# Performance work log

Measured on AMD Instinct MI355X. Metric: run time of the kernel, lower is better.

## Reference

```python
import jax, jax.numpy as jnp
import numpy as np

B, IN_CH, OUT_CH, T, N_STATE, FACTOR = 8, 128, 128, 16384, 256, 2
DT = 1.0
LN_EPS = 1e-5


def setup_inputs() -> dict:
    key = jax.random.key(0)
    k = jax.random.split(key, 5)
    x = jax.random.normal(k[0], (B, IN_CH, T), jnp.float32)
    raw_lambda = jnp.zeros((N_STATE,), jnp.float32)
    B_c = jax.random.normal(k[1], (IN_CH, N_STATE), jnp.float32) * (1.0 / np.sqrt(IN_CH))
    C_mat = jax.random.normal(k[2], (N_STATE, OUT_CH), jnp.float32) * (1.0 / np.sqrt(N_STATE))
    ln_gamma = jnp.ones((OUT_CH,), jnp.float32)
    ln_beta = jnp.zeros((OUT_CH,), jnp.float32)
    # Conv1d(out_ch*factor, out_ch, kernel_size=1): weight (out, in), bias (out,)
    W = jax.random.normal(k[3], (OUT_CH, OUT_CH * FACTOR), jnp.float32) * (1.0 / np.sqrt(OUT_CH * FACTOR))
    b = jax.random.normal(k[4], (OUT_CH,), jnp.float32) * 0.01
    return {"x": x, "raw_lambda": raw_lambda, "B_c": B_c, "C_mat": C_mat,
            "ln_gamma": ln_gamma, "ln_beta": ln_beta, "W": W, "b": b}


def reference(x, raw_lambda, B_c, C_mat, ln_gamma, ln_beta, W, b):
    # --- SSMLayerZOH ---
    lam = -jax.nn.softplus(raw_lambda)              # (N,) continuous diag, < 0
    A_d = jnp.exp(lam * DT)                         # ZOH discretized diag
    B_d = B_c * ((A_d - 1.0) / lam)[None, :]        # (IN, N)
    v = jnp.einsum('bct,cn->tbn', x, B_d)           # per-step input injection

    def step(s, vt):
        s = s * A_d + vt
        return s, s

    s0 = jnp.zeros((x.shape[0], lam.shape[0]), x.dtype)
    _, ss = jax.lax.scan(step, s0, v)               # (T, B, N)
    y = jnp.einsum('tbn,no->bto', ss, C_mat)        # (B, T, OUT)

    # --- LayerNorm(out_ch) + SiLU ---
    mu = jnp.mean(y, axis=-1, keepdims=True)
    var = jnp.mean((y - mu) ** 2, axis=-1, keepdims=True)
    h = (y - mu) / jnp.sqrt(var + LN_EPS) * ln_gamma + ln_beta
    h = h * jax.nn.sigmoid(h)                       # SiLU

    # --- Resample (factor > 1 branch): downsample T, stack factor into channels ---
    h = jnp.transpose(h, (0, 2, 1))                 # (B, OUT, T)
    Bn, C, Tt = h.shape
    hr = h.reshape(Bn, C, Tt // FACTOR, FACTOR)
    hr = jnp.transpose(hr, (0, 1, 3, 2)).reshape(Bn, C * FACTOR, Tt // FACTOR)
    out = jnp.einsum('bct,oc->bot', hr, W) + b[None, :, None]  # conv1x1
    return out
```

## Files before the change

kernel.cpp:

```cpp
#include <hip/hip_runtime.h>

#define BATCH 8
#define CIN 128
#define OCH 128
#define T_LEN 16384
#define NS 256
#define CHUNK 64
#define NCHUNK (T_LEN / CHUNK)
#define THALF (T_LEN / 2)
#define SCHUNK 8192
#define HROW 132
#define NCHK 4

typedef __attribute__((ext_vector_type(8))) short bf16x8;
typedef __attribute__((ext_vector_type(4))) float f32x4;
typedef __attribute__((ext_vector_type(4))) unsigned int u32x4;

__device__ __forceinline__ unsigned int pk2(float lo, float hi) {
  unsigned int d;
  asm("v_cvt_pk_bf16_f32 %0, %1, %2" : "=v"(d) : "v"(lo), "v"(hi));
  return d;
}
__device__ __forceinline__ unsigned short f2bf(float f) {
  unsigned int u = __float_as_uint(f);
  u += 0x7fffu + ((u >> 16) & 1u);
  return (unsigned short)(u >> 16);
}
__device__ __forceinline__ float softplusf_(float v) {
  return (v > 20.0f) ? v : log1pf(expf(v));
}
__device__ __forceinline__ void rawbar() {
  __builtin_amdgcn_sched_barrier(0);
  asm volatile("s_waitcnt lgkmcnt(0)" ::: "memory");
  __builtin_amdgcn_sched_barrier(0);
  __builtin_amdgcn_s_barrier();
  __builtin_amdgcn_sched_barrier(0);
}

__global__ __launch_bounds__(256) void k_prep(
    const float* __restrict__ rl, const float* __restrict__ Bc,
    const float* __restrict__ Cm, const float* __restrict__ W,
    unsigned short* __restrict__ BdT, unsigned short* __restrict__ CT,
    unsigned short* __restrict__ Wb, float* __restrict__ Ad, float* __restrict__ rL,
    float* __restrict__ PWf)
{
  const int tid = blockIdx.x * 256 + threadIdx.x;
  if (tid < NS * CIN) {
    const int n = tid >> 7, c = tid & 127;
    float lam = -softplusf_(rl[n]);
    float ad = expf(lam);
    float sc = (ad - 1.0f) / lam;
    BdT[tid] = f2bf(Bc[c * NS + n] * sc);
  } else if (tid < 2 * NS * CIN) {
    const int i = tid - NS * CIN;
    const int o = i >> 8, n = i & 255;
    CT[i] = f2bf(Cm[n * OCH + o]);
  } else if (tid < 3 * NS * CIN) {
    const int i = tid - 2 * NS * CIN;
    Wb[i] = f2bf(W[i]);
  } else if (tid < 3 * NS * CIN + NS) {
    const int n = tid - 3 * NS * CIN;
    float lam = -softplusf_(rl[n]);
    Ad[n] = expf(lam);
    rL[n] = expf(lam * (float)CHUNK);
  } else if (tid < 3 * NS * CIN + NS + 32 * NS) {
    const int i = tid - (3 * NS * CIN + NS);
    const int tp = i >> 8, n = i & 255;
    float lam = -softplusf_(rl[n]);
    PWf[i] = expf(lam * (float)(2 * tp + 1));
  }
}

__global__ __launch_bounds__(256) void k_combine(float* __restrict__ carry,
                                                 const float* __restrict__ rL)
{
  const int b = blockIdx.x >> 3;
  const int ng = blockIdx.x & 7;
  const int t = threadIdx.x;
  __shared__ float Y[32][NCHUNK];
  float* base = carry + ((size_t)b * NCHUNK + t) * NS + ng * 32;
  #pragma unroll
  for (int i4 = 0; i4 < 8; ++i4) {
    float4 q = *(const float4*)(base + i4 * 4);
    Y[i4 * 4 + 0][t] = q.x; Y[i4 * 4 + 1][t] = q.y;
    Y[i4 * 4 + 2][t] = q.z; Y[i4 * 4 + 3][t] = q.w;
  }
  float rp[32];
  #pragma unroll
  for (int i = 0; i < 32; ++i) rp[i] = rL[ng * 32 + i];
  __syncthreads();
  for (int d = 1; d < NCHUNK; d <<= 1) {
    float tmp[32];
    #pragma unroll
    for (int i = 0; i < 32; ++i) tmp[i] = (t >= d) ? Y[i][t - d] : 0.0f;
    __syncthreads();
    #pragma unroll
    for (int i = 0; i < 32; ++i) { Y[i][t] += rp[i] * tmp[i]; rp[i] *= rp[i]; }
    __syncthreads();
  }
  const int tm = (t == 0) ? 0 : (t - 1);
  #pragma unroll
  for (int i4 = 0; i4 < 8; ++i4) {
    float a = Y[i4 * 4 + 0][tm], bb = Y[i4 * 4 + 1][tm];
    float c = Y[i4 * 4 + 2][tm], dd = Y[i4 * 4 + 3][tm];
    float4 q;
    q.x = (t == 0) ? 0.0f : a;  q.y = (t == 0) ? 0.0f : bb;
    q.z = (t == 0) ? 0.0f : c;  q.w = (t == 0) ? 0.0f : dd;
    *(float4*)(base + i4 * 4) = q;
  }
}

__global__ __launch_bounds__(512, 4) void k_scan(
    const float* __restrict__ x,
    const unsigned short* __restrict__ BdT,
    const float* __restrict__ Ad,
    unsigned int* __restrict__ s0,
    float* __restrict__ carry)
{
  const int bid = blockIdx.x;
  const int b = bid >> 8;
  const int kc = bid & 255;
  const int tid = threadIdx.x;
  const int w = tid >> 6, l = tid & 63, l15 = l & 15, g = l >> 4;

  __shared__ __align__(16) unsigned int Xt[64 * 64];

  {
    const int c2 = w * 8 + (l & 7);
    const int t0b = (l >> 3) * 8;
    const float* r0 = x + ((size_t)(b * CIN + 2 * c2)) * T_LEN + kc * CHUNK + t0b;
    const f32x4 xa0 = *(const f32x4*)r0;
    const f32x4 xa1 = *(const f32x4*)(r0 + 4);
    const f32x4 xb0 = *(const f32x4*)(r0 + T_LEN);
    const f32x4 xb1 = *(const f32x4*)(r0 + T_LEN + 4);
    #pragma unroll
    for (int k = 0; k < 8; ++k) {
      const int t = t0b + k;
      const float va = (k < 4) ? xa0[k & 3] : xa1[k & 3];
      const float vb = (k < 4) ? xb0[k & 3] : xb1[k & 3];
      Xt[t * 64 + (c2 ^ ((t & 7) << 2))] = pk2(va, vb);
    }
  }

  bf16x8 Bf[2][4];
  #pragma unroll
  for (int nt = 0; nt < 2; ++nt)
    #pragma unroll
    for (int kt = 0; kt < 4; ++kt)
      Bf[nt][kt] = *(const bf16x8*)&BdT[(w * 32 + nt * 16 + l15) * CIN + kt * 32 + g * 8];

  float A1[2], A2[2], A3[2], A4[2], A8[2], A16[2], A4G[2], M1[2], M2[2];
  #pragma unroll
  for (int nt = 0; nt < 2; ++nt) {
    const float a1 = Ad[w * 32 + nt * 16 + l15];
    A1[nt] = a1; A2[nt] = a1 * a1; A3[nt] = A2[nt] * a1; A4[nt] = A2[nt] * A2[nt];
    A8[nt] = A4[nt] * A4[nt]; A16[nt] = A8[nt] * A8[nt];
    float a4g = 1.0f;
    if (g & 1) a4g *= A4[nt];
    if (g & 2) a4g *= A8[nt];
    A4G[nt] = a4g;
    M1[nt] = (g >= 1) ? A4[nt] : 0.0f;
    M2[nt] = (g >= 2) ? A8[nt] : 0.0f;
  }
  __syncthreads();

  f32x4 vac[4][2] = {};
  #pragma unroll
  for (int kt = 0; kt < 4; ++kt) {
    bf16x8 afr[4];
    #pragma unroll
    for (int mt = 0; mt < 4; ++mt)
      afr[mt] = *(const bf16x8*)&Xt[(mt * 16 + l15) * 64 + ((kt * 16 + g * 4) ^ ((l15 & 7) << 2))];
    #pragma unroll
    for (int nt = 0; nt < 2; ++nt)
      #pragma unroll
      for (int mt = 0; mt < 4; ++mt)
        vac[mt][nt] = __builtin_amdgcn_mfma_f32_16x16x32_bf16(afr[mt], Bf[nt][kt], vac[mt][nt], 0, 0, 0);
  }

  float crv[2];
  #pragma unroll
  for (int nt = 0; nt < 2; ++nt) {
    float cr = 0.0f;
    #pragma unroll
    for (int mt = 0; mt < 4; ++mt) {
      const float p0 = vac[mt][nt][0];
      const float p1 = fmaf(A1[nt], p0, vac[mt][nt][1]);
      const float p2 = fmaf(A1[nt], p1, vac[mt][nt][2]);
      const float p3 = fmaf(A1[nt], p2, vac[mt][nt][3]);
      float c0 = p3;
      float u = __shfl_up(c0, 16);
      c0 = fmaf(M1[nt], u, c0);
      u = __shfl_up(c0, 32);
      c0 = fmaf(M2[nt], u, c0);
      float e = __shfl_up(c0, 16);
      e = (g == 0) ? 0.0f : e;
      const float seed = fmaf(A4G[nt], cr, e);
      vac[mt][nt][0] = fmaf(A1[nt], seed, p0);
      vac[mt][nt][1] = fmaf(A2[nt], seed, p1);
      vac[mt][nt][2] = fmaf(A3[nt], seed, p2);
      vac[mt][nt][3] = fmaf(A4[nt], seed, p3);
      const float ctop = __shfl(c0, 48 + l15);
      cr = fmaf(A16[nt], cr, ctop);
    }
    crv[nt] = cr;
  }

  unsigned int* sc = s0 + (size_t)(b * NCHUNK + kc) * SCHUNK;
  #pragma unroll
  for (int mt = 0; mt < 4; ++mt)
    #pragma unroll
    for (int nt = 0; nt < 2; ++nt) {
      const int n = w * 32 + nt * 16 + l15;
      #pragma unroll
      for (int rp = 0; rp < 2; ++rp) {
        const int tp = mt * 8 + g * 2 + rp;
        sc[tp * 256 + n] = pk2(vac[mt][nt][rp * 2], vac[mt][nt][rp * 2 + 1]);
      }
    }
  if (g == 0) {
    #pragma unroll
    for (int nt = 0; nt < 2; ++nt)
      carry[((size_t)b * NCHUNK + kc) * NS + (w * 32 + nt * 16 + l15)] = crv[nt];
  }
}

__global__ __launch_bounds__(512, 2) void k_apply(
    const unsigned int* __restrict__ S,
    const unsigned short* __restrict__ CT,
    const unsigned short* __restrict__ Wb,
    const float* __restrict__ PWf,
    const float* __restrict__ Ad,
    const float* __restrict__ carry,
    const float* __restrict__ lng, const float* __restrict__ lnb,
    const float* __restrict__ bias,
    float* __restrict__ out)
{
  const int bid = blockIdx.x;
  const int b = bid / (NCHUNK / NCHK);
  const int kc0 = (bid % (NCHUNK / NCHK)) * NCHK;
  const int tid = threadIdx.x;
  const int w = tid >> 6, l = tid & 63, l15 = l & 15, g = l >> 4;
  const int tt = w >> 2, oq = w & 3;

  __shared__ __align__(16) unsigned short V2[64 * 256];
  __shared__ __align__(16) unsigned int Hr[32 * HROW];
  __shared__ __align__(16) float Lexf[64 * 8];

  const f32x4 adv = *(const f32x4*)&Ad[4 * l];

  bf16x8 ctf[8][2];
  #pragma unroll
  for (int kt = 0; kt < 8; ++kt)
    #pragma unroll
    for (int ot = 0; ot < 2; ++ot)
      ctf[kt][ot] = *(const bf16x8*)&CT[(oq * 32 + ot * 16 + l15) * NS + kt * 32 + g * 8];
  bf16x8 wf[8];
  #pragma unroll
  for (int kt = 0; kt < 8; ++kt)
    wf[kt] = *(const bf16x8*)&Wb[(w * 16 + l15) * NS + kt * 32 + g * 8];
  f32x4 pwv[4];
  #pragma unroll
  for (int r = 0; r < 4; ++r)
    pwv[r] = *(const f32x4*)&PWf[(r * 8 + w) * 256 + 4 * l];
  const float ga0 = lng[oq * 32 + l15],      be0 = lnb[oq * 32 + l15];
  const float ga1 = lng[oq * 32 + 16 + l15], be1 = lnb[oq * 32 + 16 + l15];
  const float bia = bias[w * 16 + l15];

  u32x4 st0, st1, st2, st3;
  f32x4 sd;

#define LOAD_ST(KC) do {                                                    \
    const unsigned int* scb_ = S + (size_t)(b * NCHUNK + (KC)) * SCHUNK;    \
    st0 = *(const u32x4*)&scb_[0 * 2048 + tid * 4];                         \
    st1 = *(const u32x4*)&scb_[1 * 2048 + tid * 4];                         \
    st2 = *(const u32x4*)&scb_[2 * 2048 + tid * 4];                         \
    st3 = *(const u32x4*)&scb_[3 * 2048 + tid * 4];                         \
    sd  = *(const f32x4*)&carry[((size_t)b * NCHUNK + (KC)) * NS + 4 * l];  \
  } while (0)

#define CORRECT_ROW(QV, RR) do {                                            \
    const float e00 = sd[0] * pwv[RR][0];                                   \
    const float e01 = sd[1] * pwv[RR][1];                                   \
    const float e02 = sd[2] * pwv[RR][2];                                   \
    const float e03 = sd[3] * pwv[RR][3];                                   \
    const float lo0 = __uint_as_float(QV[0] << 16) + e00;                   \
    const float hi0 = __uint_as_float(QV[0] & 0xffff0000u) + e00 * adv[0];  \
    const float lo1 = __uint_as_float(QV[1] << 16) + e01;                   \
    const float hi1 = __uint_as_float(QV[1] & 0xffff0000u) + e01 * adv[1];  \
    const float lo2 = __uint_as_float(QV[2] << 16) + e02;                   \
    const float hi2 = __uint_as_float(QV[2] & 0xffff0000u) + e02 * adv[2];  \
    const float lo3 = __uint_as_float(QV[3] << 16) + e03;                   \
    const float hi3 = __uint_as_float(QV[3] & 0xffff0000u) + e03 * adv[3];  \
    const int t0_ = ((RR) * 8 + w) * 2;                                     \
    const int t1_ = t0_ + 1;                                                \
    uint2 wlo; wlo.x = pk2(lo0, lo1); wlo.y = pk2(lo2, lo3);                \
    uint2 whi; whi.x = pk2(hi0, hi1); whi.y = pk2(hi2, hi3);                \
    *(uint2*)&V2[t0_ * 256 + ((((l >> 1) ^ ((t0_ & 7) << 2)) << 3) | ((l & 1) << 2))] = wlo; \
    *(uint2*)&V2[t1_ * 256 + ((((l >> 1) ^ ((t1_ & 7) << 2)) << 3) | ((l & 1) << 2))] = whi; \
  } while (0)

#define CORRECT_STORE() do {                                                \
    CORRECT_ROW(st0, 0);                                                    \
    CORRECT_ROW(st1, 1);                                                    \
    CORRECT_ROW(st2, 2);                                                    \
    CORRECT_ROW(st3, 3);                                                    \
  } while (0)

  LOAD_ST(kc0);
  CORRECT_STORE();
  LOAD_ST(kc0 + 1);
  rawbar();

  #pragma unroll 1
  for (int i = 0; i < NCHK; ++i) {
    const int kc = kc0 + i;

    f32x4 yac[2][2] = {};
    #pragma unroll
    for (int kt = 0; kt < 8; ++kt) {
      bf16x8 As[2];
      #pragma unroll
      for (int mt = 0; mt < 2; ++mt) {
        const int t = tt * 32 + mt * 16 + l15;
        As[mt] = *(const bf16x8*)&V2[t * 256 + (((kt * 4 + g) ^ ((t & 7) << 2)) << 3)];
      }
      #pragma unroll
      for (int ot = 0; ot < 2; ++ot)
        #pragma unroll
        for (int mt = 0; mt < 2; ++mt)
          yac[mt][ot] = __builtin_amdgcn_mfma_f32_16x16x32_bf16(As[mt], ctf[kt][ot], yac[mt][ot], 0, 0, 0);
    }
    #pragma unroll
    for (int mt = 0; mt < 2; ++mt)
      #pragma unroll
      for (int r = 0; r < 4; ++r) {
        float s1 = yac[mt][0][r] + yac[mt][1][r];
        float s2 = yac[mt][0][r] * yac[mt][0][r] + yac[mt][1][r] * yac[mt][1][r];
        #pragma unroll
        for (int d = 1; d < 16; d <<= 1) { s1 += __shfl_xor(s1, d); s2 += __shfl_xor(s2, d); }
        if (l15 == 0) {
          const int t = tt * 32 + mt * 16 + g * 4 + r;
          *(float2*)&Lexf[t * 8 + oq * 2] = make_float2(s1, s2);
        }
      }
    rawbar();

    #pragma unroll
    for (int mt = 0; mt < 2; ++mt) {
      float mu[4], rs[4];
      #pragma unroll
      for (int r = 0; r < 4; ++r) {
        const int t = tt * 32 + mt * 16 + g * 4 + r;
        const float4 f0 = *(const float4*)&Lexf[t * 8];
        const float4 f1 = *(const float4*)&Lexf[t * 8 + 4];
        const float m = (f0.x + f0.z + f1.x + f1.z) * (1.0f / 128.0f);
        const float va = (f0.y + f0.w + f1.y + f1.w) * (1.0f / 128.0f) - m * m;
        mu[r] = m;
        rs[r] = rsqrtf(va + 1e-5f);
      }
      #pragma unroll
      for (int ot = 0; ot < 2; ++ot) {
        const int o = oq * 32 + ot * 16 + l15;
        const float ga = ot ? ga1 : ga0;
        const float be = ot ? be1 : be0;
        #pragma unroll
        for (int rp = 0; rp < 2; ++rp) {
          float h0 = (yac[mt][ot][rp * 2] - mu[rp * 2]) * rs[rp * 2] * ga + be;
          h0 = h0 * __builtin_amdgcn_rcpf(1.0f + __expf(-h0));
          float h1 = (yac[mt][ot][rp * 2 + 1] - mu[rp * 2 + 1]) * rs[rp * 2 + 1] * ga + be;
          h1 = h1 * __builtin_amdgcn_rcpf(1.0f + __expf(-h1));
          const int t2 = tt * 16 + mt * 8 + g * 2 + rp;
          Hr[t2 * HROW + o] = pk2(h0, h1);
        }
      }
    }
    if (i + 1 < NCHK) {
      CORRECT_STORE();
      if (i + 2 < NCHK) LOAD_ST(kc + 2);
    }
    rawbar();

    {
      f32x4 oac[2] = {};
      #pragma unroll
      for (int kt = 0; kt < 8; ++kt) {
        bf16x8 Aa0, Aa1;
        {
          union { bf16x8 v; u32x4 u; } Ax;
          Ax.u = *(const u32x4*)&Hr[(l15) * HROW + kt * 16 + g * 4];
          Aa0 = Ax.v;
          Ax.u = *(const u32x4*)&Hr[(16 + l15) * HROW + kt * 16 + g * 4];
          Aa1 = Ax.v;
        }
        oac[0] = __builtin_amdgcn_mfma_f32_16x16x32_bf16(Aa0, wf[kt], oac[0], 0, 0, 0);
        oac[1] = __builtin_amdgcn_mfma_f32_16x16x32_bf16(Aa1, wf[kt], oac[1], 0, 0, 0);
      }
      const int o = w * 16 + l15;
      #pragma unroll
      for (int mt = 0; mt < 2; ++mt) {
        float4 q;
        q.x = oac[mt][0] + bia;
        q.y = oac[mt][1] + bia;
        q.z = oac[mt][2] + bia;
        q.w = oac[mt][3] + bia;
        *(float4*)(out + ((size_t)(b * OCH + o)) * THALF + kc * 32 + mt * 16 + g * 4) = q;
      }
    }
  }
#undef LOAD_ST
#undef CORRECT_ROW
#undef CORRECT_STORE
}

extern "C" void kernel_launch(void* const* d_in, const int* in_sizes, int n_in,
                              void* d_out, int out_size, void* d_ws, size_t ws_size,
                              hipStream_t stream) {
  const float* x    = (const float*)d_in[0];
  const float* rl   = (const float*)d_in[1];
  const float* Bc   = (const float*)d_in[2];
  const float* Cm   = (const float*)d_in[3];
  const float* lng  = (const float*)d_in[4];
  const float* lnb  = (const float*)d_in[5];
  const float* W    = (const float*)d_in[6];
  const float* bias = (const float*)d_in[7];
  float* out = (float*)d_out;

  char* ws = (char*)d_ws;
  unsigned short* BdT = (unsigned short*)(ws);
  unsigned short* CT  = (unsigned short*)(ws + 65536);
  unsigned short* Wb  = (unsigned short*)(ws + 131072);
  float* Ad    = (float*)(ws + 196608);
  float* rL    = (float*)(ws + 197632);
  float* PWf   = (float*)(ws + 198656);
  float* carry = (float*)(ws + 231424);
  unsigned int* S = (unsigned int*)(ws + 231424 + 2097152);

  k_prep<<<417, 256, 0, stream>>>(rl, Bc, Cm, W, BdT, CT, Wb, Ad, rL, PWf);
  k_scan<<<BATCH * NCHUNK, 512, 0, stream>>>(x, BdT, Ad, S, carry);
  k_combine<<<64, 256, 0, stream>>>(carry, rL);
  k_apply<<<BATCH * (NCHUNK / NCHK), 512, 0, stream>>>(S, CT, Wb, PWf, Ad, carry,
                                                       lng, lnb, bias, out);
}
```

Before: 101.8 us.

## Process two chunks per iteration in k_apply with doubled LDS buffers

Doubles the chunks per block (NCHK 4→8) and processes two chunks per loop iteration using separate V2/Hr/Lexf buffers. This halves the barriers per chunk and exposes more independent MFMA work between syncs. In exchange it uses more LDS and registers, which may cut occupancy below the launch-bounds target, and launches half as many blocks.

```diff
diff --git a/kernel.cpp b/kernel.cpp
--- a/kernel.cpp
+++ b/kernel.cpp
@@ -10,7 +10,7 @@
 #define THALF (T_LEN / 2)
 #define SCHUNK 8192
 #define HROW 132
-#define NCHK 4
+#define NCHK 8
 
 typedef __attribute__((ext_vector_type(8))) short bf16x8;
 typedef __attribute__((ext_vector_type(4))) float f32x4;
@@ -243,9 +243,11 @@
   const int w = tid >> 6, l = tid & 63, l15 = l & 15, g = l >> 4;
   const int tt = w >> 2, oq = w & 3;
 
-  __shared__ __align__(16) unsigned short V2[64 * 256];
-  __shared__ __align__(16) unsigned int Hr[32 * HROW];
-  __shared__ __align__(16) float Lexf[64 * 8];
+  __shared__ __align__(16) unsigned short V2a[64 * 256];
+  __shared__ __align__(16) unsigned short V2b[64 * 256];
+  __shared__ __align__(16) unsigned int Hra[32 * HROW];
+  __shared__ __align__(16) unsigned int Hrb[32 * HROW];
+  __shared__ __align__(16) float Lexf[2][64 * 8];
 
   const f32x4 adv = *(const f32x4*)&Ad[4 * l];
 
@@ -267,23 +269,23 @@
   const float ga1 = lng[oq * 32 + 16 + l15], be1 = lnb[oq * 32 + 16 + l15];
   const float bia = bias[w * 16 + l15];
 
-  u32x4 st0, st1, st2, st3;
-  f32x4 sd;
-
-#define LOAD_ST(KC) do {                                                    \
+  u32x4 sa0, sa1, sa2, sa3, sb0, sb1, sb2, sb3;
+  f32x4 sda, sdb;
+
+#define LOAD_ST(KC, T0, T1, T2, T3, SD) do {                                \
     const unsigned int* scb_ = S + (size_t)(b * NCHUNK + (KC)) * SCHUNK;    \
-    st0 = *(const u32x4*)&scb_[0 * 2048 + tid * 4];                         \
-    st1 = *(const u32x4*)&scb_[1 * 2048 + tid * 4];                         \
-    st2 = *(const u32x4*)&scb_[2 * 2048 + tid * 4];                         \
-    st3 = *(const u32x4*)&scb_[3 * 2048 + tid * 4];                         \
-    sd  = *(const f32x4*)&carry[((size_t)b * NCHUNK + (KC)) * NS + 4 * l];  \
-  } while (0)
-
-#define CORRECT_ROW(QV, RR) do {                                            \
-    const float e00 = sd[0] * pwv[RR][0];                                   \
-    const float e01 = sd[1] * pwv[RR][1];                                   \
-    const float e02 = sd[2] * pwv[RR][2];                                   \
-    const float e03 = sd[3] * pwv[RR][3];                                   \
+    T0 = *(const u32x4*)&scb_[0 * 2048 + tid * 4];                          \
+    T1 = *(const u32x4*)&scb_[1 * 2048 + tid * 4];                          \
+    T2 = *(const u32x4*)&scb_[2 * 2048 + tid * 4];                          \
+    T3 = *(const u32x4*)&scb_[3 * 2048 + tid * 4];                          \
+    SD = *(const f32x4*)&carry[((size_t)b * NCHUNK + (KC)) * NS + 4 * l];   \
+  } while (0)
+
+#define CORRECT_ROW(DSTV, QV, RR, SD) do {                                  \
+    const float e00 = SD[0] * pwv[RR][0];                                   \
+    const float e01 = SD[1] * pwv[RR][1];                                   \
+    const float e02 = SD[2] * pwv[RR][2];                                   \
+    const float e03 = SD[3] * pwv[RR][3];                                   \
     const float lo0 = __uint_as_float(QV[0] << 16) + e00;                   \
     const float hi0 = __uint_as_float(QV[0] & 0xffff0000u) + e00 * adv[0];  \
     const float lo1 = __uint_as_float(QV[1] << 16) + e01;                   \
@@ -296,121 +298,146 @@
     const int t1_ = t0_ + 1;                                                \
     uint2 wlo; wlo.x = pk2(lo0, lo1); wlo.y = pk2(lo2, lo3);                \
     uint2 whi; whi.x = pk2(hi0, hi1); whi.y = pk2(hi2, hi3);                \
-    *(uint2*)&V2[t0_ * 256 + ((((l >> 1) ^ ((t0_ & 7) << 2)) << 3) | ((l & 1) << 2))] = wlo; \
-    *(uint2*)&V2[t1_ * 256 + ((((l >> 1) ^ ((t1_ & 7) << 2)) << 3) | ((l & 1) << 2))] = whi; \
-  } while (0)
-
-#define CORRECT_STORE() do {                                                \
-    CORRECT_ROW(st0, 0);                                                    \
-    CORRECT_ROW(st1, 1);                                                    \
-    CORRECT_ROW(st2, 2);                                                    \
-    CORRECT_ROW(st3, 3);                                                    \
-  } while (0)
-
-  LOAD_ST(kc0);
-  CORRECT_STORE();
-  LOAD_ST(kc0 + 1);
+    *(uint2*)&DSTV[t0_ * 256 + ((((l >> 1) ^ ((t0_ & 7) << 2)) << 3) | ((l & 1) << 2))] = wlo; \
+    *(uint2*)&DSTV[t1_ * 256 + ((((l >> 1) ^ ((t1_ & 7) << 2)) << 3) | ((l & 1) << 2))] = whi; \
+  } while (0)
+
+#define CORRECT_STORE(DSTV, T0, T1, T2, T3, SD) do {                        \
+    CORRECT_ROW(DSTV, T0, 0, SD);                                           \
+    CORRECT_ROW(DSTV, T1, 1, SD);                                           \
+    CORRECT_ROW(DSTV, T2, 2, SD);                                           \
+    CORRECT_ROW(DSTV, T3, 3, SD);                                           \
+  } while (0)
+
+#define YGEMM(V2X, YAC, IDX) do {                                           \
+    _Pragma("unroll")                                                       \
+    for (int kt = 0; kt < 8; ++kt) {                                        \
+      bf16x8 As0, As1;                                                      \
+      {                                                                     \
+        const int t0 = tt * 32 + l15;                                       \
+        As0 = *(const bf16x8*)&V2X[t0 * 256 + (((kt * 4 + g) ^ ((t0 & 7) << 2)) << 3)]; \
+        const int t1 = tt * 32 + 16 + l15;                                  \
+        As1 = *(const bf16x8*)&V2X[t1 * 256 + (((kt * 4 + g) ^ ((t1 & 7) << 2)) << 3)]; \
+      }                                                                     \
+      _Pragma("unroll")                                                     \
+      for (int ot = 0; ot < 2; ++ot) {                                      \
+        YAC[0][ot] = __builtin_amdgcn_mfma_f32_16x16x32_bf16(As0, ctf[kt][ot], YAC[0][ot], 0, 0, 0); \
+        YAC[1][ot] = __builtin_amdgcn_mfma_f32_16x16x32_bf16(As1, ctf[kt][ot], YAC[1][ot], 0, 0, 0); \
+      }                                                                     \
+    }                                                                       \
+    _Pragma("unroll")                                                       \
+    for (int mt = 0; mt < 2; ++mt)                                          \
+      _Pragma("unroll")                                                     \
+      for (int r = 0; r < 4; ++r) {                                         \
+        float s1 = YAC[mt][0][r] + YAC[mt][1][r];                           \
+        float s2 = YAC[mt][0][r] * YAC[mt][0][r] + YAC[mt][1][r] * YAC[mt][1][r]; \
+        _Pragma("unroll")                                                   \
+        for (int d = 1; d < 16; d <<= 1) { s1 += __shfl_xor(s1, d); s2 += __shfl_xor(s2, d); } \
+        if (l15 == 0) {                                                     \
+          const int t = tt * 32 + mt * 16 + g * 4 + r;                      \
+          *(float2*)&Lexf[IDX][t * 8 + oq * 2] = make_float2(s1, s2);       \
+        }                                                                   \
+      }                                                                     \
+  } while (0)
+
+#define LNSILU(HRX, YAC, IDX) do {                                          \
+    _Pragma("unroll")                                                       \
+    for (int mt = 0; mt < 2; ++mt) {                                        \
+      float mu[4], rs[4];                                                   \
+      _Pragma("unroll")                                                     \
+      for (int r = 0; r < 4; ++r) {                                         \
+        const int t = tt * 32 + mt * 16 + g * 4 + r;                        \
+        const float4 f0 = *(const float4*)&Lexf[IDX][t * 8];                \
+        const float4 f1 = *(const float4*)&Lexf[IDX][t * 8 + 4];            \
+        const float m = (f0.x + f0.z + f1.x + f1.z) * (1.0f / 128.0f);      \
+        const float va = (f0.y + f0.w + f1.y + f1.w) * (1.0f / 128.0f) - m * m; \
+        mu[r] = m;                                                          \
+        rs[r] = rsqrtf(va + 1e-5f);                                         \
+      }                                                                     \
+      _Pragma("unroll")                                                     \
+      for (int ot = 0; ot < 2; ++ot) {                                      \
+        const int o = oq * 32 + ot * 16 + l15;                              \
+        const float ga = ot ? ga1 : ga0;                                    \
+        const float be = ot ? be1 : be0;                                    \
+        _Pragma("unroll")                                                   \
+        for (int rp = 0; rp < 2; ++rp) {                                    \
+          float h0 = (YAC[mt][ot][rp * 2] - mu[rp * 2]) * rs[rp * 2] * ga + be; \
+          h0 = h0 * __builtin_amdgcn_rcpf(1.0f + __expf(-h0));              \
+          float h1 = (YAC[mt][ot][rp * 2 + 1] - mu[rp * 2 + 1]) * rs[rp * 2 + 1] * ga + be; \
+          h1 = h1 * __builtin_amdgcn_rcpf(1.0f + __expf(-h1));              \
+          const int t2 = tt * 16 + mt * 8 + g * 2 + rp;                     \
+          HRX[t2 * HROW + o] = pk2(h0, h1);                                 \
+        }                                                                   \
+      }                                                                     \
+    }                                                                       \
+  } while (0)
+
+#define OUTGEMM(HRX, KC) do {                                               \
+    f32x4 oac0 = {}, oac1 = {};                                             \
+    _Pragma("unroll")                                                       \
+    for (int kt = 0; kt < 8; ++kt) {                                        \
+      bf16x8 Aa0, Aa1;                                                      \
+      {                                                                     \
+        union { bf16x8 v; u32x4 u; } Ax;                                    \
+        Ax.u = *(const u32x4*)&HRX[(l15) * HROW + kt * 16 + g * 4];         \
+        Aa0 = Ax.v;                                                         \
+        Ax.u = *(const u32x4*)&HRX[(16 + l15) * HROW + kt * 16 + g * 4];    \
+        Aa1 = Ax.v;                                                         \
+      }                                                                     \
+      oac0 = __builtin_amdgcn_mfma_f32_16x16x32_bf16(Aa0, wf[kt], oac0, 0, 0, 0); \
+      oac1 = __builtin_amdgcn_mfma_f32_16x16x32_bf16(Aa1, wf[kt], oac1, 0, 0, 0); \
+    }                                                                       \
+    const int o = w * 16 + l15;                                             \
+    float4 q0;                                                              \
+    q0.x = oac0[0] + bia; q0.y = oac0[1] + bia;                             \
+    q0.z = oac0[2] + bia; q0.w = oac0[3] + bia;                             \
+    *(float4*)(out + ((size_t)(b * OCH + o)) * THALF + (KC) * 32 + g * 4) = q0; \
+    float4 q1;                                                              \
+    q1.x = oac1[0] + bia; q1.y = oac1[1] + bia;                             \
+    q1.z = oac1[2] + bia; q1.w = oac1[3] + bia;                             \
+    *(float4*)(out + ((size_t)(b * OCH + o)) * THALF + (KC) * 32 + 16 + g * 4) = q1; \
+  } while (0)
+
+  LOAD_ST(kc0 + 0, sa0, sa1, sa2, sa3, sda);
+  CORRECT_STORE(V2a, sa0, sa1, sa2, sa3, sda);
+  LOAD_ST(kc0 + 1, sb0, sb1, sb2, sb3, sdb);
+  CORRECT_STORE(V2b, sb0, sb1, sb2, sb3, sdb);
+  LOAD_ST(kc0 + 2, sa0, sa1, sa2, sa3, sda);
+  LOAD_ST(kc0 + 3, sb0, sb1, sb2, sb3, sdb);
   rawbar();
 
   #pragma unroll 1
-  for (int i = 0; i < NCHK; ++i) {
-    const int kc = kc0 + i;
-
-    f32x4 yac[2][2] = {};
-    #pragma unroll
-    for (int kt = 0; kt < 8; ++kt) {
-      bf16x8 As[2];
-      #pragma unroll
-      for (int mt = 0; mt < 2; ++mt) {
-        const int t = tt * 32 + mt * 16 + l15;
-        As[mt] = *(const bf16x8*)&V2[t * 256 + (((kt * 4 + g) ^ ((t & 7) << 2)) << 3)];
-      }
-      #pragma unroll
-      for (int ot = 0; ot < 2; ++ot)
-        #pragma unroll
-        for (int mt = 0; mt < 2; ++mt)
-          yac[mt][ot] = __builtin_amdgcn_mfma_f32_16x16x32_bf16(As[mt], ctf[kt][ot], yac[mt][ot], 0, 0, 0);
-    }
-    #pragma unroll
-    for (int mt = 0; mt < 2; ++mt)
-      #pragma unroll
-      for (int r = 0; r < 4; ++r) {
-        float s1 = yac[mt][0][r] + yac[mt][1][r];
-        float s2 = yac[mt][0][r] * yac[mt][0][r] + yac[mt][1][r] * yac[mt][1][r];
-        #pragma unroll
-        for (int d = 1; d < 16; d <<= 1) { s1 += __shfl_xor(s1, d); s2 += __shfl_xor(s2, d); }
-        if (l15 == 0) {
-          const int t = tt * 32 + mt * 16 + g * 4 + r;
-          *(float2*)&Lexf[t * 8 + oq * 2] = make_float2(s1, s2);
-        }
-      }
+  for (int i = 0; i < NCHK / 2; ++i) {
+    const int kcA = kc0 + 2 * i;
+    const int kcB = kcA + 1;
+
+    f32x4 yacA[2][2] = {};
+    f32x4 yacB[2][2] = {};
+    YGEMM(V2a, yacA, 0);
+    YGEMM(V2b, yacB, 1);
     rawbar();
 
-    #pragma unroll
-    for (int mt = 0; mt < 2; ++mt) {
-      float mu[4], rs[4];
-      #pragma unroll
-      for (int r = 0; r < 4; ++r) {
-        const int t = tt * 32 + mt * 16 + g * 4 + r;
-        const float4 f0 = *(const float4*)&Lexf[t * 8];
-        const float4 f1 = *(const float4*)&Lexf[t * 8 + 4];
-        const float m = (f0.x + f0.z + f1.x + f1.z) * (1.0f / 128.0f);
-        const float va = (f0.y + f0.w + f1.y + f1.w) * (1.0f / 128.0f) - m * m;
-        mu[r] = m;
-        rs[r] = rsqrtf(va + 1e-5f);
-      }
-      #pragma unroll
-      for (int ot = 0; ot < 2; ++ot) {
-        const int o = oq * 32 + ot * 16 + l15;
-        const float ga = ot ? ga1 : ga0;
-        const float be = ot ? be1 : be0;
-        #pragma unroll
-        for (int rp = 0; rp < 2; ++rp) {
-          float h0 = (yac[mt][ot][rp * 2] - mu[rp * 2]) * rs[rp * 2] * ga + be;
-          h0 = h0 * __builtin_amdgcn_rcpf(1.0f + __expf(-h0));
-          float h1 = (yac[mt][ot][rp * 2 + 1] - mu[rp * 2 + 1]) * rs[rp * 2 + 1] * ga + be;
-          h1 = h1 * __builtin_amdgcn_rcpf(1.0f + __expf(-h1));
-          const int t2 = tt * 16 + mt * 8 + g * 2 + rp;
-          Hr[t2 * HROW + o] = pk2(h0, h1);
-        }
+    LNSILU(Hra, yacA, 0);
+    LNSILU(Hrb, yacB, 1);
+    if (i + 1 < NCHK / 2) {
+      CORRECT_STORE(V2a, sa0, sa1, sa2, sa3, sda);
+      CORRECT_STORE(V2b, sb0, sb1, sb2, sb3, sdb);
+      if (i + 2 < NCHK / 2) {
+        LOAD_ST(kcA + 4, sa0, sa1, sa2, sa3, sda);
+        LOAD_ST(kcB + 4, sb0, sb1, sb2, sb3, sdb);
       }
     }
-    if (i + 1 < NCHK) {
-      CORRECT_STORE();
-      if (i + 2 < NCHK) LOAD_ST(kc + 2);
-    }
     rawbar();
 
-    {
-      f32x4 oac[2] = {};
-      #pragma unroll
-      for (int kt = 0; kt < 8; ++kt) {
-        bf16x8 Aa0, Aa1;
-        {
-          union { bf16x8 v; u32x4 u; } Ax;
-          Ax.u = *(const u32x4*)&Hr[(l15) * HROW + kt * 16 + g * 4];
-          Aa0 = Ax.v;
-          Ax.u = *(const u32x4*)&Hr[(16 + l15) * HROW + kt * 16 + g * 4];
-          Aa1 = Ax.v;
-        }
-        oac[0] = __builtin_amdgcn_mfma_f32_16x16x32_bf16(Aa0, wf[kt], oac[0], 0, 0, 0);
-        oac[1] = __builtin_amdgcn_mfma_f32_16x16x32_bf16(Aa1, wf[kt], oac[1], 0, 0, 0);
-      }
-      const int o = w * 16 + l15;
-      #pragma unroll
-      for (int mt = 0; mt < 2; ++mt) {
-        float4 q;
-        q.x = oac[mt][0] + bia;
-        q.y = oac[mt][1] + bia;
-        q.z = oac[mt][2] + bia;
-        q.w = oac[mt][3] + bia;
-        *(float4*)(out + ((size_t)(b * OCH + o)) * THALF + kc * 32 + mt * 16 + g * 4) = q;
-      }
-    }
+    OUTGEMM(Hra, kcA);
+    OUTGEMM(Hrb, kcB);
   }
 #undef LOAD_ST
 #undef CORRECT_ROW
 #undef CORRECT_STORE
+#undef YGEMM
+#undef LNSILU
+#undef OUTGEMM
 }
 
 extern "C" void kernel_launch(void* const* d_in, const int* in_sizes, int n_in,
```

Measured after the change: 97.64 us. -4.0%, faster.

## Halve k_apply block to 4 waves, each covering all 64 timesteps

Applied to the files above, without the earlier changes.

The apply kernel now runs with 256 threads (4 waves) instead of 512. Each wave handles the full 64-row time tile and a 32-wide output slice, with twice as many MFMA tiles, state loads and correction rows per wave. This cuts the number of waves that share the C/W fragments and the per-wave redundancy, but it doubles register pressure (wf, pwv, st, yac arrays) and may lower occupancy or cause spills.

```diff
diff --git a/kernel.cpp b/kernel.cpp
--- a/kernel.cpp
+++ b/kernel.cpp
@@ -225,7 +225,7 @@
   }
 }
 
-__global__ __launch_bounds__(512, 2) void k_apply(
+__global__ __launch_bounds__(256, 2) void k_apply(
     const unsigned int* __restrict__ S,
     const unsigned short* __restrict__ CT,
     const unsigned short* __restrict__ Wb,
@@ -241,7 +241,6 @@
   const int kc0 = (bid % (NCHUNK / NCHK)) * NCHK;
   const int tid = threadIdx.x;
   const int w = tid >> 6, l = tid & 63, l15 = l & 15, g = l >> 4;
-  const int tt = w >> 2, oq = w & 3;
 
   __shared__ __align__(16) unsigned short V2[64 * 256];
   __shared__ __align__(16) unsigned int Hr[32 * HROW];
@@ -254,28 +253,35 @@
   for (int kt = 0; kt < 8; ++kt)
     #pragma unroll
     for (int ot = 0; ot < 2; ++ot)
-      ctf[kt][ot] = *(const bf16x8*)&CT[(oq * 32 + ot * 16 + l15) * NS + kt * 32 + g * 8];
-  bf16x8 wf[8];
-  #pragma unroll
-  for (int kt = 0; kt < 8; ++kt)
-    wf[kt] = *(const bf16x8*)&Wb[(w * 16 + l15) * NS + kt * 32 + g * 8];
-  f32x4 pwv[4];
-  #pragma unroll
-  for (int r = 0; r < 4; ++r)
-    pwv[r] = *(const f32x4*)&PWf[(r * 8 + w) * 256 + 4 * l];
-  const float ga0 = lng[oq * 32 + l15],      be0 = lnb[oq * 32 + l15];
-  const float ga1 = lng[oq * 32 + 16 + l15], be1 = lnb[oq * 32 + 16 + l15];
-  const float bia = bias[w * 16 + l15];
-
-  u32x4 st0, st1, st2, st3;
+      ctf[kt][ot] = *(const bf16x8*)&CT[(w * 32 + ot * 16 + l15) * NS + kt * 32 + g * 8];
+  bf16x8 wf[2][8];
+  #pragma unroll
+  for (int nt = 0; nt < 2; ++nt)
+    #pragma unroll
+    for (int kt = 0; kt < 8; ++kt)
+      wf[nt][kt] = *(const bf16x8*)&Wb[(w * 32 + nt * 16 + l15) * NS + kt * 32 + g * 8];
+  f32x4 pwv[8];
+  #pragma unroll
+  for (int r = 0; r < 8; ++r)
+    pwv[r] = *(const f32x4*)&PWf[(r * 4 + w) * 256 + 4 * l];
+  const float ga0 = lng[w * 32 + l15],      be0 = lnb[w * 32 + l15];
+  const float ga1 = lng[w * 32 + 16 + l15], be1 = lnb[w * 32 + 16 + l15];
+  const float bia0 = bias[w * 32 + l15];
+  const float bia1 = bias[w * 32 + 16 + l15];
+
+  u32x4 st0, st1, st2, st3, st4, st5, st6, st7;
   f32x4 sd;
 
 #define LOAD_ST(KC) do {                                                    \
     const unsigned int* scb_ = S + (size_t)(b * NCHUNK + (KC)) * SCHUNK;    \
-    st0 = *(const u32x4*)&scb_[0 * 2048 + tid * 4];                         \
-    st1 = *(const u32x4*)&scb_[1 * 2048 + tid * 4];                         \
-    st2 = *(const u32x4*)&scb_[2 * 2048 + tid * 4];                         \
-    st3 = *(const u32x4*)&scb_[3 * 2048 + tid * 4];                         \
+    st0 = *(const u32x4*)&scb_[0 * 1024 + tid * 4];                         \
+    st1 = *(const u32x4*)&scb_[1 * 1024 + tid * 4];                         \
+    st2 = *(const u32x4*)&scb_[2 * 1024 + tid * 4];                         \
+    st3 = *(const u32x4*)&scb_[3 * 1024 + tid * 4];                         \
+    st4 = *(const u32x4*)&scb_[4 * 1024 + tid * 4];                         \
+    st5 = *(const u32x4*)&scb_[5 * 1024 + tid * 4];                         \
+    st6 = *(const u32x4*)&scb_[6 * 1024 + tid * 4];                         \
+    st7 = *(const u32x4*)&scb_[7 * 1024 + tid * 4];                         \
     sd  = *(const f32x4*)&carry[((size_t)b * NCHUNK + (KC)) * NS + 4 * l];  \
   } while (0)
 
@@ -292,7 +298,7 @@
     const float hi2 = __uint_as_float(QV[2] & 0xffff0000u) + e02 * adv[2];  \
     const float lo3 = __uint_as_float(QV[3] << 16) + e03;                   \
     const float hi3 = __uint_as_float(QV[3] & 0xffff0000u) + e03 * adv[3];  \
-    const int t0_ = ((RR) * 8 + w) * 2;                                     \
+    const int t0_ = ((RR) * 4 + w) * 2;                                     \
     const int t1_ = t0_ + 1;                                                \
     uint2 wlo; wlo.x = pk2(lo0, lo1); wlo.y = pk2(lo2, lo3);                \
     uint2 whi; whi.x = pk2(hi0, hi1); whi.y = pk2(hi2, hi3);                \
@@ -301,10 +307,10 @@
   } while (0)
 
 #define CORRECT_STORE() do {                                                \
-    CORRECT_ROW(st0, 0);                                                    \
-    CORRECT_ROW(st1, 1);                                                    \
-    CORRECT_ROW(st2, 2);                                                    \
-    CORRECT_ROW(st3, 3);                                                    \
+    CORRECT_ROW(st0, 0); CORRECT_ROW(st1, 1);                               \
+    CORRECT_ROW(st2, 2); CORRECT_ROW(st3, 3);                               \
+    CORRECT_ROW(st4, 4); CORRECT_ROW(st5, 5);                               \
+    CORRECT_ROW(st6, 6); CORRECT_ROW(st7, 7);                               \
   } while (0)
 
   LOAD_ST(kc0);
@@ -316,23 +322,23 @@
   for (int i = 0; i < NCHK; ++i) {
     const int kc = kc0 + i;
 
-    f32x4 yac[2][2] = {};
+    f32x4 yac[4][2] = {};
     #pragma unroll
     for (int kt = 0; kt < 8; ++kt) {
-      bf16x8 As[2];
-      #pragma unroll
-      for (int mt = 0; mt < 2; ++mt) {
-        const int t = tt * 32 + mt * 16 + l15;
+      bf16x8 As[4];
+      #pragma unroll
+      for (int mt = 0; mt < 4; ++mt) {
+        const int t = mt * 16 + l15;
         As[mt] = *(const bf16x8*)&V2[t * 256 + (((kt * 4 + g) ^ ((t & 7) << 2)) << 3)];
       }
       #pragma unroll
       for (int ot = 0; ot < 2; ++ot)
         #pragma unroll
-        for (int mt = 0; mt < 2; ++mt)
+        for (int mt = 0; mt < 4; ++mt)
           yac[mt][ot] = __builtin_amdgcn_mfma_f32_16x16x32_bf16(As[mt], ctf[kt][ot], yac[mt][ot], 0, 0, 0);
     }
     #pragma unroll
-    for (int mt = 0; mt < 2; ++mt)
+    for (int mt = 0; mt < 4; ++mt)
       #pragma unroll
       for (int r = 0; r < 4; ++r) {
         float s1 = yac[mt][0][r] + yac[mt][1][r];
@@ -340,18 +346,18 @@
         #pragma unroll
         for (int d = 1; d < 16; d <<= 1) { s1 += __shfl_xor(s1, d); s2 += __shfl_xor(s2, d); }
         if (l15 == 0) {
-          const int t = tt * 32 + mt * 16 + g * 4 + r;
-          *(float2*)&Lexf[t * 8 + oq * 2] = make_float2(s1, s2);
+          const int t = mt * 16 + g * 4 + r;
+          *(float2*)&Lexf[t * 8 + w * 2] = make_float2(s1, s2);
         }
       }
     rawbar();
 
     #pragma unroll
-    for (int mt = 0; mt < 2; ++mt) {
+    for (int mt = 0; mt < 4; ++mt) {
       float mu[4], rs[4];
       #pragma unroll
       for (int r = 0; r < 4; ++r) {
-        const int t = tt * 32 + mt * 16 + g * 4 + r;
+        const int t = mt * 16 + g * 4 + r;
         const float4 f0 = *(const float4*)&Lexf[t * 8];
         const float4 f1 = *(const float4*)&Lexf[t * 8 + 4];
         const float m = (f0.x + f0.z + f1.x + f1.z) * (1.0f / 128.0f);
@@ -361,7 +367,7 @@
       }
       #pragma unroll
       for (int ot = 0; ot < 2; ++ot) {
-        const int o = oq * 32 + ot * 16 + l15;
+        const int o = w * 32 + ot * 16 + l15;
         const float ga = ot ? ga1 : ga0;
         const float be = ot ? be1 : be0;
         #pragma unroll
@@ -370,7 +376,7 @@
           h0 = h0 * __builtin_amdgcn_rcpf(1.0f + __expf(-h0));
           float h1 = (yac[mt][ot][rp * 2 + 1] - mu[rp * 2 + 1]) * rs[rp * 2 + 1] * ga + be;
           h1 = h1 * __builtin_amdgcn_rcpf(1.0f + __expf(-h1));
-          const int t2 = tt * 16 + mt * 8 + g * 2 + rp;
+          const int t2 = mt * 8 + g * 2 + rp;
           Hr[t2 * HROW + o] = pk2(h0, h1);
         }
       }
@@ -382,7 +388,7 @@
     rawbar();
 
     {
-      f32x4 oac[2] = {};
+      f32x4 oac[2][2] = {};
       #pragma unroll
       for (int kt = 0; kt < 8; ++kt) {
         bf16x8 Aa0, Aa1;
@@ -393,18 +399,25 @@
           Ax.u = *(const u32x4*)&Hr[(16 + l15) * HROW + kt * 16 + g * 4];
           Aa1 = Ax.v;
         }
-        oac[0] = __builtin_amdgcn_mfma_f32_16x16x32_bf16(Aa0, wf[kt], oac[0], 0, 0, 0);
-        oac[1] = __builtin_amdgcn_mfma_f32_16x16x32_bf16(Aa1, wf[kt], oac[1], 0, 0, 0);
-      }
-      const int o = w * 16 + l15;
-      #pragma unroll
-      for (int mt = 0; mt < 2; ++mt) {
-        float4 q;
-        q.x = oac[mt][0] + bia;
-        q.y = oac[mt][1] + bia;
-        q.z = oac[mt][2] + bia;
-        q.w = oac[mt][3] + bia;
-        *(float4*)(out + ((size_t)(b * OCH + o)) * THALF + kc * 32 + mt * 16 + g * 4) = q;
+        #pragma unroll
+        for (int nt = 0; nt < 2; ++nt) {
+          oac[0][nt] = __builtin_amdgcn_mfma_f32_16x16x32_bf16(Aa0, wf[nt][kt], oac[0][nt], 0, 0, 0);
+          oac[1][nt] = __builtin_amdgcn_mfma_f32_16x16x32_bf16(Aa1, wf[nt][kt], oac[1][nt], 0, 0, 0);
+        }
+      }
+      #pragma unroll
+      for (int nt = 0; nt < 2; ++nt) {
+        const int o = w * 32 + nt * 16 + l15;
+        const float bia = nt ? bia1 : bia0;
+        #pragma unroll
+        for (int mt = 0; mt < 2; ++mt) {
+          float4 q;
+          q.x = oac[mt][nt][0] + bia;
+          q.y = oac[mt][nt][1] + bia;
+          q.z = oac[mt][nt][2] + bia;
+          q.w = oac[mt][nt][3] + bia;
+          *(float4*)(out + ((size_t)(b * OCH + o)) * THALF + kc * 32 + mt * 16 + g * 4) = q;
+        }
       }
     }
   }
@@ -439,6 +452,6 @@
   k_prep<<<417, 256, 0, stream>>>(rl, Bc, Cm, W, BdT, CT, Wb, Ad, rL, PWf);
   k_scan<<<BATCH * NCHUNK, 512, 0, stream>>>(x, BdT, Ad, S, carry);
   k_combine<<<64, 256, 0, stream>>>(carry, rL);
-  k_apply<<<BATCH * (NCHUNK / NCHK), 512, 0, stream>>>(S, CT, Wb, PWf, Ad, carry,
+  k_apply<<<BATCH * (NCHUNK / NCHK), 256, 0, stream>>>(S, CT, Wb, PWf, Ad, carry,
                                                        lng, lnb, bias, out);
 }
```

Result: slower. 112.4 us (+10.5%).
